# Optimization experiments

Measured on AMD Instinct MI355X. Metric: run time of the kernel, lower is better.

The kernel has to match this reference:

```python
import jax, jax.numpy as jnp
import numpy as np

NB_COMP = 8
LAT_DIM = 512
NB_NEUR = 1024
OUT_DIM = 512
N_SAMPLES = 16384


def setup_inputs() -> dict:
    key = jax.random.key(0)
    ks = jax.random.split(key, 8)
    s1 = 1.0 / np.sqrt(LAT_DIM)
    s2 = 1.0 / np.sqrt(NB_NEUR)
    return {
        "epsilon": jax.random.normal(ks[0], (N_SAMPLES, LAT_DIM), dtype=jnp.float32),
        "comp_idx": jax.random.randint(ks[1], (N_SAMPLES,), 0, NB_COMP, dtype=jnp.int32),
        "mu": jnp.zeros((NB_COMP, LAT_DIM), dtype=jnp.float32),
        "rho": jnp.zeros((NB_COMP,), dtype=jnp.float32),  # sigma = softplus(rho)
        "W1": jax.random.normal(ks[2], (NB_COMP, LAT_DIM, NB_NEUR), dtype=jnp.float32) * s1,
        "b1": jax.random.normal(ks[3], (NB_COMP, NB_NEUR), dtype=jnp.float32) * s1,
        "W2": jax.random.normal(ks[4], (NB_COMP, NB_NEUR, OUT_DIM), dtype=jnp.float32) * s2,
        "b2": jax.random.normal(ks[5], (NB_COMP, OUT_DIM), dtype=jnp.float32) * s2,
    }


def reference(epsilon, comp_idx, mu, rho, W1, b1, W2, b2):
    # GNNens.forward: per-sample categorical component dispatch through a
    # 1-hidden-layer sigmoid MLP. Vectorized as compute-all-components + select.
    sigma = jax.nn.softplus(rho)                          # [C]
    # lat_c[c,n,d] = epsilon[n,d] * sigma[c] + mu[c,d]
    lat = epsilon[None, :, :] * sigma[:, None, None] + mu[:, None, :]  # [C,N,D]
    h = jax.nn.sigmoid(jnp.einsum('cnd,cdh->cnh', lat, W1) + b1[:, None, :])  # [C,N,H]
    y = jnp.einsum('cnh,cho->cno', h, W2) + b2[:, None, :]                    # [C,N,O]
    # select each sample's routed component
    idx = comp_idx[None, :, None].astype(jnp.int32)       # [1,N,1]
    out = jnp.take_along_axis(y, idx, axis=0)[0]          # [N,O]
    return out
```

## Files before the change

### kernel.cpp

```cpp
#include <hip/hip_runtime.h>
#include <stdint.h>

#define NCOMP 8
#define LATD  512
#define HID   1024
#define OUTD  512
#define NS    16384

typedef unsigned short u16;
typedef __bf16 bf16x8 __attribute__((ext_vector_type(8)));
typedef float  f32x4  __attribute__((ext_vector_type(4)));

#define ORDER_OFF  256
#define APACK_OFF  (ORDER_OFF + NS*4)
#define W1T_OFF    (APACK_OFF + (size_t)NS*LATD*2)
#define W2T_OFF    (W1T_OFF + (size_t)NCOMP*LATD*HID*2)
#define H_OFF      (W2T_OFF + (size_t)NCOMP*HID*OUTD*2)
#define WS_NEEDED  (H_OFF + (size_t)NS*HID*2)

__device__ __forceinline__ u16 f2b(float f) {
  unsigned int u = __builtin_bit_cast(unsigned int, f);
  u = (u + 0x7FFFu + ((u >> 16) & 1u)) >> 16;
  return (u16)u;
}

__device__ __forceinline__ void load_lds16(const void* g, void* l) {
  __builtin_amdgcn_global_load_lds((const __attribute__((address_space(1))) void*)g,
                                   (__attribute__((address_space(3))) void*)l, 16, 0, 0);
}

__global__ void k_count(const int* __restrict__ idx, int* __restrict__ counts) {
  __shared__ int h[NCOMP];
  int t = threadIdx.x;
  if (t < NCOMP) h[t] = 0;
  __syncthreads();
  int n = blockIdx.x*256 + t;
  if (n < NS) atomicAdd(&h[idx[n]], 1);
  __syncthreads();
  if (t < NCOMP) atomicAdd(&counts[t], h[t]);
}

__global__ void k_scan(const int* __restrict__ counts, int* __restrict__ offsets,
                       const float* __restrict__ rho, float* __restrict__ sigma) {
  if (threadIdx.x == 0) {
    int acc = 0;
    for (int c = 0; c < NCOMP; ++c) { offsets[c] = acc; acc += counts[c]; }
    offsets[NCOMP] = acc;
  }
  if (threadIdx.x < NCOMP) {
    float r = rho[threadIdx.x];
    sigma[threadIdx.x] = (r > 20.f) ? r : log1pf(expf(r));
  }
}

__global__ void k_scatter(const int* __restrict__ idx, const int* __restrict__ offsets,
                          int* __restrict__ cursors, int* __restrict__ order) {
  __shared__ int lh[NCOMP];
  __shared__ int lbase[NCOMP];
  int t = threadIdx.x;
  if (t < NCOMP) lh[t] = 0;
  __syncthreads();
  int n = blockIdx.x*256 + t;
  int c = 0, rank = 0;
  if (n < NS) { c = idx[n]; rank = atomicAdd(&lh[c], 1); }
  __syncthreads();
  if (t < NCOMP) lbase[t] = atomicAdd(&cursors[t], lh[t]);
  __syncthreads();
  if (n < NS) order[offsets[c] + lbase[c] + rank] = n;
}

__global__ void k_pack(const float* __restrict__ eps, const int* __restrict__ idx,
                       const float* __restrict__ mu, const float* __restrict__ sigma,
                       const int* __restrict__ order, u16* __restrict__ Apack) {
  int g = blockIdx.x*256 + threadIdx.x;
  int i = g >> 6;
  int d = (g & 63) << 3;
  if (i >= NS) return;
  int s = order[i];
  int c = idx[s];
  float sg = sigma[c];
  const float4* ep = reinterpret_cast<const float4*>(eps + (size_t)s*LATD + d);
  const float4* mp = reinterpret_cast<const float4*>(mu  + (size_t)c*LATD + d);
  float4 e0 = ep[0], e1 = ep[1], m0 = mp[0], m1 = mp[1];
  unsigned o0 = f2b(e0.x*sg+m0.x), o1 = f2b(e0.y*sg+m0.y), o2 = f2b(e0.z*sg+m0.z), o3 = f2b(e0.w*sg+m0.w);
  unsigned o4 = f2b(e1.x*sg+m1.x), o5 = f2b(e1.y*sg+m1.y), o6 = f2b(e1.z*sg+m1.z), o7 = f2b(e1.w*sg+m1.w);
  uint4 pk;
  pk.x = o0 | (o1<<16); pk.y = o2 | (o3<<16); pk.z = o4 | (o5<<16); pk.w = o6 | (o7<<16);
  *reinterpret_cast<uint4*>(Apack + (size_t)i*LATD + d) = pk;
}

template<int R, int CC>
__global__ void k_transpose(const float* __restrict__ W, u16* __restrict__ WT) {
  __shared__ float tile[64][65];
  int c  = blockIdx.z;
  int r0 = blockIdx.y*64, c0 = blockIdx.x*64;
  const float* src = W  + (size_t)c*R*CC;
  u16*        dst  = WT + (size_t)c*R*CC;
  int tx = threadIdx.x & 63, ty = threadIdx.x >> 6;
  for (int rr = ty; rr < 64; rr += 4)
    tile[rr][tx] = src[(size_t)(r0+rr)*CC + c0 + tx];
  __syncthreads();
  for (int rr = ty; rr < 64; rr += 4)
    dst[(size_t)(c0+rr)*R + r0 + tx] = f2b(tile[tx][rr]);
}

template<int K, int NB, int STAGE>
__global__ __launch_bounds__(256, 2)
void k_gemm(const u16* __restrict__ A, const u16* __restrict__ BT,
            const int* __restrict__ offsets, const int* __restrict__ order,
            const float* __restrict__ bias,
            u16* __restrict__ Hout, float* __restrict__ Yout) {
  __shared__ u16 As[128*64];
  __shared__ u16 Bs[128*64];
  __shared__ int ord[128];

  const int c = blockIdx.z;
  const int bstart = offsets[c];
  const int bend   = offsets[c+1];
  const int tile0  = bstart + blockIdx.y*128;
  if (tile0 >= bend) return;
  const int ncol0 = blockIdx.x*128;

  const int tid  = threadIdx.x;
  const int wave = tid >> 6;
  const int lane = tid & 63;
  const int srow = (wave<<5) + (lane>>3);
  const int scol = (lane&7)<<3;

  if (STAGE == 2 && tid < 128) {
    int gr = tile0 + tid;
    ord[tid] = order[gr < bend ? gr : bstart];
  }

  size_t a_off[4], b_off[4];
  const size_t bbase = (size_t)c * NB * K;
  #pragma unroll
  for (int i = 0; i < 4; ++i) {
    int ar = tile0 + srow + (i<<3);
    if (ar >= bend) ar = bend - 1;
    a_off[i] = (size_t)ar * K + scol;
    b_off[i] = bbase + (size_t)(ncol0 + srow + (i<<3)) * K + scol;
  }

  const int wr   = (wave >> 1) << 6;
  const int wc   = (wave & 1) << 6;
  const int quad = lane >> 4;
  const int l16  = lane & 15;

  float bcol[4];
  #pragma unroll
  for (int ni = 0; ni < 4; ++ni)
    bcol[ni] = bias[(size_t)c*NB + ncol0 + wc + (ni<<4) + l16];

  f32x4 acc[4][4] = {};

  for (int k0 = 0; k0 < K; k0 += 64) {
    #pragma unroll
    for (int i = 0; i < 4; ++i)
      load_lds16(A + a_off[i] + k0, &As[((wave<<5) + (i<<3))<<6]);
    #pragma unroll
    for (int i = 0; i < 4; ++i)
      load_lds16(BT + b_off[i] + k0, &Bs[((wave<<5) + (i<<3))<<6]);
    __syncthreads();
    #pragma unroll
    for (int kk = 0; kk < 64; kk += 32) {
      bf16x8 af[4], bfr[4];
      #pragma unroll
      for (int mi = 0; mi < 4; ++mi)
        af[mi] = *reinterpret_cast<const bf16x8*>(&As[((wr + (mi<<4) + l16)<<6) + kk + (quad<<3)]);
      #pragma unroll
      for (int ni = 0; ni < 4; ++ni)
        bfr[ni] = *reinterpret_cast<const bf16x8*>(&Bs[((wc + (ni<<4) + l16)<<6) + kk + (quad<<3)]);
      #pragma unroll
      for (int mi = 0; mi < 4; ++mi)
        #pragma unroll
        for (int ni = 0; ni < 4; ++ni)
          acc[mi][ni] = __builtin_amdgcn_mfma_f32_16x16x32_bf16(af[mi], bfr[ni], acc[mi][ni], 0, 0, 0);
    }
    __syncthreads();
  }

  #pragma unroll
  for (int mi = 0; mi < 4; ++mi) {
    #pragma unroll
    for (int r = 0; r < 4; ++r) {
      const int row_l = wr + (mi<<4) + (quad<<2) + r;
      const int grow  = tile0 + row_l;
      if (grow < bend) {
        #pragma unroll
        for (int ni = 0; ni < 4; ++ni) {
          const int col = ncol0 + wc + (ni<<4) + l16;
          float v = acc[mi][ni][r] + bcol[ni];
          if (STAGE == 1) {
            v = 1.0f / (1.0f + __expf(-v));
            Hout[(size_t)grow*NB + col] = f2b(v);
          } else {
            Yout[(size_t)ord[row_l]*NB + col] = v;
          }
        }
      }
    }
  }
}

__global__ void k_naive(const float* __restrict__ eps, const int* __restrict__ idx,
                        const float* __restrict__ mu, const float* __restrict__ rho,
                        const float* __restrict__ W1, const float* __restrict__ b1,
                        const float* __restrict__ W2, const float* __restrict__ b2,
                        float* __restrict__ out) {
  __shared__ float lat[LATD];
  __shared__ float h[HID];
  int n = blockIdx.x, t = threadIdx.x;
  int c = idx[n];
  float r = rho[c];
  float sg = (r > 20.f) ? r : log1pf(expf(r));
  for (int d = t; d < LATD; d += 256) lat[d] = eps[(size_t)n*LATD+d]*sg + mu[(size_t)c*LATD+d];
  __syncthreads();
  for (int j = t; j < HID; j += 256) {
    float a = b1[(size_t)c*HID+j];
    const float* w = W1 + (size_t)c*LATD*HID + j;
    for (int d = 0; d < LATD; ++d) a += lat[d]*w[(size_t)d*HID];
    h[j] = 1.f/(1.f+expf(-a));
  }
  __syncthreads();
  for (int o = t; o < OUTD; o += 256) {
    float a = b2[(size_t)c*OUTD+o];
    const float* w = W2 + (size_t)c*HID*OUTD + o;
    for (int j = 0; j < HID; ++j) a += h[j]*w[(size_t)j*OUTD];
    out[(size_t)n*OUTD+o] = a;
  }
}

extern "C" void kernel_launch(void* const* d_in, const int* in_sizes, int n_in,
                              void* d_out, int out_size, void* d_ws, size_t ws_size,
                              hipStream_t stream) {
  const float* eps = (const float*)d_in[0];
  const int*   idx = (const int*)d_in[1];
  const float* mu  = (const float*)d_in[2];
  const float* rho = (const float*)d_in[3];
  const float* W1  = (const float*)d_in[4];
  const float* b1  = (const float*)d_in[5];
  const float* W2  = (const float*)d_in[6];
  const float* b2  = (const float*)d_in[7];
  float* out = (float*)d_out;

  if (ws_size < WS_NEEDED) {
    k_naive<<<NS, 256, 0, stream>>>(eps, idx, mu, rho, W1, b1, W2, b2, out);
    return;
  }

  char* ws = (char*)d_ws;
  int*   counts  = (int*)(ws + 0);
  int*   cursors = (int*)(ws + 32);
  int*   offsets = (int*)(ws + 64);
  float* sigma   = (float*)(ws + 128);
  int*   order   = (int*)(ws + ORDER_OFF);
  u16*   Apack   = (u16*)(ws + APACK_OFF);
  u16*   W1T     = (u16*)(ws + W1T_OFF);
  u16*   W2T     = (u16*)(ws + W2T_OFF);
  u16*   Hws     = (u16*)(ws + H_OFF);

  hipMemsetAsync(ws, 0, 256, stream);
  k_count  <<<64, 256, 0, stream>>>(idx, counts);
  k_scan   <<<1, 64, 0, stream>>>(counts, offsets, rho, sigma);
  k_scatter<<<64, 256, 0, stream>>>(idx, offsets, cursors, order);
  k_pack   <<<NS*64/256, 256, 0, stream>>>(eps, idx, mu, sigma, order, Apack);
  k_transpose<LATD, HID><<<dim3(HID/64, LATD/64, NCOMP), 256, 0, stream>>>(W1, W1T);
  k_transpose<HID, OUTD><<<dim3(OUTD/64, HID/64, NCOMP), 256, 0, stream>>>(W2, W2T);
  k_gemm<LATD, HID, 1><<<dim3(HID/128, NS/128, NCOMP), 256, 0, stream>>>(
      Apack, W1T, offsets, order, b1, Hws, nullptr);
  k_gemm<HID, OUTD, 2><<<dim3(OUTD/128, NS/128, NCOMP), 256, 0, stream>>>(
      Hws, W2T, offsets, order, b2, nullptr, out);
}
```

Baseline: 217.7 us.

## Fuse bucketing into one kernel, compact tile map, retile GEMMs, merge transposes

Replaces the memset plus count/scan/scatter sequence with a single-block bucketing kernel that also builds compact per-stage tile maps. Both weight transposes are merged into one launch. The GEMMs now index a dense tile list instead of a full NS/128 x NCOMP grid, so they no longer launch many blocks that exit immediately. Tile shapes change to 64x128 for stage 1 and 128x64 for stage 2, which gives more blocks on the hardware. In exchange, the single-block bucket kernel serialises the index processing and the smaller tiles lower per-block data reuse.

Measured after the change: 232.0 us. +6.5%, slower.

```diff
diff --git a/kernel.cpp b/kernel.cpp
--- a/kernel.cpp
+++ b/kernel.cpp
@@ -11,7 +11,9 @@
 typedef __bf16 bf16x8 __attribute__((ext_vector_type(8)));
 typedef float  f32x4  __attribute__((ext_vector_type(4)));
 
-#define ORDER_OFF  256
+#define MAP1_SLOTS (NS/64 + NCOMP)
+#define MAP2_SLOTS (NS/128 + NCOMP)
+#define ORDER_OFF  2048
 #define APACK_OFF  (ORDER_OFF + NS*4)
 #define W1T_OFF    (APACK_OFF + (size_t)NS*LATD*2)
 #define W2T_OFF    (W1T_OFF + (size_t)NCOMP*LATD*HID*2)
@@ -29,44 +31,70 @@
                                    (__attribute__((address_space(3))) void*)l, 16, 0, 0);
 }
 
-__global__ void k_count(const int* __restrict__ idx, int* __restrict__ counts) {
-  __shared__ int h[NCOMP];
-  int t = threadIdx.x;
-  if (t < NCOMP) h[t] = 0;
-  __syncthreads();
-  int n = blockIdx.x*256 + t;
-  if (n < NS) atomicAdd(&h[idx[n]], 1);
-  __syncthreads();
-  if (t < NCOMP) atomicAdd(&counts[t], h[t]);
-}
-
-__global__ void k_scan(const int* __restrict__ counts, int* __restrict__ offsets,
-                       const float* __restrict__ rho, float* __restrict__ sigma) {
-  if (threadIdx.x == 0) {
+__global__ __launch_bounds__(1024)
+void k_bucket(const int* __restrict__ idx, const float* __restrict__ rho,
+              int* __restrict__ offsets, float* __restrict__ sigma,
+              int* __restrict__ ntiles, int* __restrict__ map1, int* __restrict__ map2,
+              int* __restrict__ order) {
+  __shared__ int cnt[NCOMP][1024];
+  __shared__ int wtot[NCOMP][16];
+  const int t = threadIdx.x;
+  const int wave = t >> 6, lane = t & 63;
+
+  int my[16];
+  #pragma unroll
+  for (int i = 0; i < 16; ++i) my[i] = idx[t + (i << 10)];
+  #pragma unroll
+  for (int c = 0; c < NCOMP; ++c) cnt[c][t] = 0;
+  #pragma unroll
+  for (int i = 0; i < 16; ++i) cnt[my[i]][t]++;
+  __syncthreads();
+
+  #pragma unroll
+  for (int c = 0; c < NCOMP; ++c) {
+    int v = cnt[c][t];
+    int s = v;
+    #pragma unroll
+    for (int d = 1; d < 64; d <<= 1) {
+      int u = __shfl_up(s, d);
+      if (lane >= d) s += u;
+    }
+    cnt[c][t] = s - v;
+    if (lane == 63) wtot[c][wave] = s;
+  }
+  __syncthreads();
+
+  if (t == 0) {
     int acc = 0;
-    for (int c = 0; c < NCOMP; ++c) { offsets[c] = acc; acc += counts[c]; }
+    int csz[NCOMP];
+    for (int c = 0; c < NCOMP; ++c) {
+      offsets[c] = acc;
+      int start = acc;
+      for (int w = 0; w < 16; ++w) { int x = wtot[c][w]; wtot[c][w] = acc; acc += x; }
+      csz[c] = acc - start;
+    }
     offsets[NCOMP] = acc;
-  }
-  if (threadIdx.x < NCOMP) {
-    float r = rho[threadIdx.x];
-    sigma[threadIdx.x] = (r > 20.f) ? r : log1pf(expf(r));
-  }
-}
-
-__global__ void k_scatter(const int* __restrict__ idx, const int* __restrict__ offsets,
-                          int* __restrict__ cursors, int* __restrict__ order) {
-  __shared__ int lh[NCOMP];
-  __shared__ int lbase[NCOMP];
-  int t = threadIdx.x;
-  if (t < NCOMP) lh[t] = 0;
-  __syncthreads();
-  int n = blockIdx.x*256 + t;
-  int c = 0, rank = 0;
-  if (n < NS) { c = idx[n]; rank = atomicAdd(&lh[c], 1); }
-  __syncthreads();
-  if (t < NCOMP) lbase[t] = atomicAdd(&cursors[t], lh[t]);
-  __syncthreads();
-  if (n < NS) order[offsets[c] + lbase[c] + rank] = n;
+    int n1 = 0, n2 = 0;
+    for (int c = 0; c < NCOMP; ++c) {
+      for (int m = 0; m < (csz[c] + 63) >> 6;  ++m) map1[n1++] = (c << 16) | m;
+      for (int m = 0; m < (csz[c] + 127) >> 7; ++m) map2[n2++] = (c << 16) | m;
+    }
+    ntiles[0] = n1; ntiles[1] = n2;
+  }
+  if (t < NCOMP) {
+    float r = rho[t];
+    sigma[t] = (r > 20.f) ? r : log1pf(expf(r));
+  }
+  __syncthreads();
+
+  #pragma unroll
+  for (int c = 0; c < NCOMP; ++c) cnt[c][t] += wtot[c][wave];
+  #pragma unroll
+  for (int i = 0; i < 16; ++i) {
+    int c = my[i];
+    int p = cnt[c][t]++;
+    order[p] = t + (i << 10);
+  }
 }
 
 __global__ void k_pack(const float* __restrict__ eps, const int* __restrict__ idx,
@@ -89,13 +117,23 @@
   *reinterpret_cast<uint4*>(Apack + (size_t)i*LATD + d) = pk;
 }
 
-template<int R, int CC>
-__global__ void k_transpose(const float* __restrict__ W, u16* __restrict__ WT) {
+__global__ void k_wtrans(const float* __restrict__ W1, const float* __restrict__ W2,
+                         u16* __restrict__ W1T, u16* __restrict__ W2T) {
   __shared__ float tile[64][65];
-  int c  = blockIdx.z;
-  int r0 = blockIdx.y*64, c0 = blockIdx.x*64;
-  const float* src = W  + (size_t)c*R*CC;
-  u16*        dst  = WT + (size_t)c*R*CC;
+  int b = blockIdx.x;
+  const float* src; u16* dst; int R, CC, r0, c0;
+  if (b < 1024) {
+    int comp = b >> 7, loc = b & 127;
+    R = LATD; CC = HID;
+    c0 = (loc & 15) << 6; r0 = (loc >> 4) << 6;
+    src = W1 + (size_t)comp*R*CC; dst = W1T + (size_t)comp*R*CC;
+  } else {
+    int bb = b - 1024;
+    int comp = bb >> 7, loc = bb & 127;
+    R = HID; CC = OUTD;
+    c0 = (loc & 7) << 6; r0 = (loc >> 3) << 6;
+    src = W2 + (size_t)comp*R*CC; dst = W2T + (size_t)comp*R*CC;
+  }
   int tx = threadIdx.x & 63, ty = threadIdx.x >> 6;
   for (int rr = ty; rr < 64; rr += 4)
     tile[rr][tx] = src[(size_t)(r0+rr)*CC + c0 + tx];
@@ -104,91 +142,97 @@
     dst[(size_t)(c0+rr)*R + r0 + tx] = f2b(tile[tx][rr]);
 }
 
-template<int K, int NB, int STAGE>
+template<int K, int NB, int TM, int TN, int STAGE>
 __global__ __launch_bounds__(256, 2)
 void k_gemm(const u16* __restrict__ A, const u16* __restrict__ BT,
-            const int* __restrict__ offsets, const int* __restrict__ order,
+            const int* __restrict__ offsets, const int* __restrict__ ntiles,
+            const int* __restrict__ map, const int* __restrict__ order,
             const float* __restrict__ bias,
             u16* __restrict__ Hout, float* __restrict__ Yout) {
-  __shared__ u16 As[128*64];
-  __shared__ u16 Bs[128*64];
-  __shared__ int ord[128];
-
-  const int c = blockIdx.z;
+  constexpr int FM = TM/32, FN = TN/32;
+  constexpr int LA = TM/32, LB = TN/32;
+  __shared__ u16 As[TM*64];
+  __shared__ u16 Bs[TN*64];
+  __shared__ int ord[TM];
+
+  const int slot = blockIdx.y;
+  if (slot >= ntiles[STAGE-1]) return;
+  const int packed = map[slot];
+  const int c      = packed >> 16;
   const int bstart = offsets[c];
   const int bend   = offsets[c+1];
-  const int tile0  = bstart + blockIdx.y*128;
-  if (tile0 >= bend) return;
-  const int ncol0 = blockIdx.x*128;
+  const int tile0  = bstart + (packed & 0xffff)*TM;
+  const int ncol0  = blockIdx.x*TN;
 
   const int tid  = threadIdx.x;
   const int wave = tid >> 6;
   const int lane = tid & 63;
-  const int srow = (wave<<5) + (lane>>3);
-  const int scol = (lane&7)<<3;
-
-  if (STAGE == 2 && tid < 128) {
+  const int scol = (lane & 7) << 3;
+
+  if (STAGE == 2 && tid < TM) {
     int gr = tile0 + tid;
     ord[tid] = order[gr < bend ? gr : bstart];
   }
 
-  size_t a_off[4], b_off[4];
+  size_t a_off[LA], b_off[LB];
   const size_t bbase = (size_t)c * NB * K;
   #pragma unroll
-  for (int i = 0; i < 4; ++i) {
-    int ar = tile0 + srow + (i<<3);
+  for (int i = 0; i < LA; ++i) {
+    int ar = tile0 + wave*(TM/4) + (i<<3) + (lane>>3);
     if (ar >= bend) ar = bend - 1;
     a_off[i] = (size_t)ar * K + scol;
-    b_off[i] = bbase + (size_t)(ncol0 + srow + (i<<3)) * K + scol;
-  }
-
-  const int wr   = (wave >> 1) << 6;
-  const int wc   = (wave & 1) << 6;
+  }
+  #pragma unroll
+  for (int i = 0; i < LB; ++i)
+    b_off[i] = bbase + (size_t)(ncol0 + wave*(TN/4) + (i<<3) + (lane>>3)) * K + scol;
+
+  const int wr   = (wave >> 1) * (TM/2);
+  const int wc   = (wave & 1) * (TN/2);
   const int quad = lane >> 4;
   const int l16  = lane & 15;
 
-  float bcol[4];
-  #pragma unroll
-  for (int ni = 0; ni < 4; ++ni)
+  float bcol[FN];
+  #pragma unroll
+  for (int ni = 0; ni < FN; ++ni)
     bcol[ni] = bias[(size_t)c*NB + ncol0 + wc + (ni<<4) + l16];
 
-  f32x4 acc[4][4] = {};
+  f32x4 acc[FM][FN] = {};
 
   for (int k0 = 0; k0 < K; k0 += 64) {
     #pragma unroll
-    for (int i = 0; i < 4; ++i)
-      load_lds16(A + a_off[i] + k0, &As[((wave<<5) + (i<<3))<<6]);
-    #pragma unroll
-    for (int i = 0; i < 4; ++i)
-      load_lds16(BT + b_off[i] + k0, &Bs[((wave<<5) + (i<<3))<<6]);
+    for (int i = 0; i < LA; ++i)
+      load_lds16(A + a_off[i] + k0, &As[(wave*(TM/4) + (i<<3))<<6]);
+    #pragma unroll
+    for (int i = 0; i < LB; ++i)
+      load_lds16(BT + b_off[i] + k0, &Bs[(wave*(TN/4) + (i<<3))<<6]);
     __syncthreads();
     #pragma unroll
     for (int kk = 0; kk < 64; kk += 32) {
-      bf16x8 af[4], bfr[4];
+      bf16x8 af[FM], bfr[FN];
       #pragma unroll
-      for (int mi = 0; mi < 4; ++mi)
+      for (int mi = 0; mi < FM; ++mi)
         af[mi] = *reinterpret_cast<const bf16x8*>(&As[((wr + (mi<<4) + l16)<<6) + kk + (quad<<3)]);
       #pragma unroll
-      for (int ni = 0; ni < 4; ++ni)
+      for (int ni = 0; ni < FN; ++ni)
         bfr[ni] = *reinterpret_cast<const bf16x8*>(&Bs[((wc + (ni<<4) + l16)<<6) + kk + (quad<<3)]);
       #pragma unroll
-      for (int mi = 0; mi < 4; ++mi)
+      for (int mi = 0; mi < FM; ++mi)
         #pragma unroll
-        for (int ni = 0; ni < 4; ++ni)
+        for (int ni = 0; ni < FN; ++ni)
           acc[mi][ni] = __builtin_amdgcn_mfma_f32_16x16x32_bf16(af[mi], bfr[ni], acc[mi][ni], 0, 0, 0);
     }
     __syncthreads();
   }
 
   #pragma unroll
-  for (int mi = 0; mi < 4; ++mi) {
+  for (int mi = 0; mi < FM; ++mi) {
     #pragma unroll
     for (int r = 0; r < 4; ++r) {
       const int row_l = wr + (mi<<4) + (quad<<2) + r;
       const int grow  = tile0 + row_l;
       if (grow < bend) {
         #pragma unroll
-        for (int ni = 0; ni < 4; ++ni) {
+        for (int ni = 0; ni < FN; ++ni) {
           const int col = ncol0 + wc + (ni<<4) + l16;
           float v = acc[mi][ni][r] + bcol[ni];
           if (STAGE == 1) {
@@ -250,25 +294,22 @@
   }
 
   char* ws = (char*)d_ws;
-  int*   counts  = (int*)(ws + 0);
-  int*   cursors = (int*)(ws + 32);
-  int*   offsets = (int*)(ws + 64);
-  float* sigma   = (float*)(ws + 128);
+  int*   offsets = (int*)(ws + 0);
+  float* sigma   = (float*)(ws + 64);
+  int*   ntiles  = (int*)(ws + 96);
+  int*   map1    = (int*)(ws + 128);
+  int*   map2    = (int*)(ws + 1280);
   int*   order   = (int*)(ws + ORDER_OFF);
   u16*   Apack   = (u16*)(ws + APACK_OFF);
   u16*   W1T     = (u16*)(ws + W1T_OFF);
   u16*   W2T     = (u16*)(ws + W2T_OFF);
   u16*   Hws     = (u16*)(ws + H_OFF);
 
-  hipMemsetAsync(ws, 0, 256, stream);
-  k_count  <<<64, 256, 0, stream>>>(idx, counts);
-  k_scan   <<<1, 64, 0, stream>>>(counts, offsets, rho, sigma);
-  k_scatter<<<64, 256, 0, stream>>>(idx, offsets, cursors, order);
-  k_pack   <<<NS*64/256, 256, 0, stream>>>(eps, idx, mu, sigma, order, Apack);
-  k_transpose<LATD, HID><<<dim3(HID/64, LATD/64, NCOMP), 256, 0, stream>>>(W1, W1T);
-  k_transpose<HID, OUTD><<<dim3(OUTD/64, HID/64, NCOMP), 256, 0, stream>>>(W2, W2T);
-  k_gemm<LATD, HID, 1><<<dim3(HID/128, NS/128, NCOMP), 256, 0, stream>>>(
-      Apack, W1T, offsets, order, b1, Hws, nullptr);
-  k_gemm<HID, OUTD, 2><<<dim3(OUTD/128, NS/128, NCOMP), 256, 0, stream>>>(
-      Hws, W2T, offsets, order, b2, nullptr, out);
-}
+  k_bucket<<<1, 1024, 0, stream>>>(idx, rho, offsets, sigma, ntiles, map1, map2, order);
+  k_pack  <<<NS*64/256, 256, 0, stream>>>(eps, idx, mu, sigma, order, Apack);
+  k_wtrans<<<2048, 256, 0, stream>>>(W1, W2, W1T, W2T);
+  k_gemm<LATD, HID, 64, 128, 1><<<dim3(HID/128, MAP1_SLOTS), 256, 0, stream>>>(
+      Apack, W1T, offsets, ntiles, map1, order, b1, Hws, nullptr);
+  k_gemm<HID, OUTD, 128, 64, 2><<<dim3(OUTD/64, MAP2_SLOTS), 256, 0, stream>>>(
+      Hws, W2T, offsets, ntiles, map2, order, b2, nullptr, out);
+}
```
